# Performance work log

Measured on AMD Instinct MI355X. Metric: run time of the kernel, lower is better.

Reference implementation:

```python
import jax, jax.numpy as jnp
import numpy as np

LAMBDA_FGW = 0.5
TAU_KL = 0.1
N_OUTER = 5
N_SINKHORN = 10
DIM = 512


def _pdist(a, b):
    # sqrt(clamp(||a-b||^2, 1e-6)) computed via expansion (avoids BxKxMxD temp)
    n2 = ((a * a).sum(-1)[:, :, None] + (b * b).sum(-1)[:, None, :]
          - 2.0 * jnp.einsum('bkd,bmd->bkm', a, b))
    return jnp.sqrt(jnp.clip(n2, 1e-6, None))


def setup_inputs() -> dict:
    key = jax.random.key(0)
    ks = jax.random.split(key, 10)
    B, K, M, D = 256, 128, 128, DIM
    inp = {
        'sq': jax.random.normal(ks[0], (B, K, D), jnp.float32),
        'sr': jax.random.normal(ks[1], (B, M, D), jnp.float32),
        'mask_q': jax.random.uniform(ks[2], (B, K), jnp.float32),
        'mask_r': jax.random.uniform(ks[3], (B, M), jnp.float32),
        'centroids_q': jax.random.normal(ks[4], (B, K, D), jnp.float32),
        'centroids_r': jax.random.normal(ks[5], (B, M, D), jnp.float32),
        'W1': jax.random.normal(ks[6], (D, D), jnp.float32) * 0.02,
        'b1': jnp.zeros((D,), jnp.float32),
        'W2': jax.random.normal(ks[7], (D, D), jnp.float32) * 0.02,
        'b2': jnp.zeros((D,), jnp.float32),
        'log_eps': jnp.asarray(np.log(0.05), jnp.float32),
    }
    return inp


def reference(sq, sr, mask_q, mask_r, centroids_q, centroids_r, W1, b1, W2, b2, log_eps):
    proj = lambda x: jax.nn.relu(x @ W1 + b1) @ W2 + b2
    pq, pr = proj(sq), proj(sr)
    C = _pdist(pq, pr)                      # [B,K,M]
    Sq = _pdist(centroids_q, centroids_q)   # [B,K,K]
    Sr = _pdist(centroids_r, centroids_r)   # [B,M,M]

    mu = mask_q / (mask_q.sum(-1, keepdims=True) + 1e-8)  # [B,K]
    nu = mask_r / (mask_r.sum(-1, keepdims=True) + 1e-8)  # [B,M]
    T = mu[:, :, None] * nu[:, None, :]

    eps = jnp.clip(jnp.exp(log_eps), 0.01, 0.5)
    rho = TAU_KL / (TAU_KL + eps)
    log_mu = jnp.log(jnp.clip(mu, 1e-8, None))
    log_nu = jnp.log(jnp.clip(nu, 1e-8, None))
    Sq2, Sr2 = Sq * Sq, Sr * Sr

    C_fgw = C
    for _ in range(N_OUTER):
        t1 = jnp.einsum('bkl,bl->bk', Sq2, T.sum(2))[:, :, None]
        t2 = jnp.einsum('bm,bmn->bn', T.sum(1), Sr2)[:, None, :]
        L_gw = t1 + t2 - 2.0 * jnp.einsum('bkl,blm->bkm', Sq, jnp.einsum('blm,bmn->bln', T, Sr))
        C_fgw = (1.0 - LAMBDA_FGW) * C + LAMBDA_FGW * L_gw
        log_K = -C_fgw / eps
        log_u = jnp.zeros_like(mu)
        log_v = jnp.zeros_like(nu)
        for _ in range(N_SINKHORN):
            log_u = rho * (log_mu - jax.nn.logsumexp(log_K + log_v[:, None, :], axis=2))
            log_v = rho * (log_nu - jax.nn.logsumexp(log_K + log_u[:, :, None], axis=1))
        T = jnp.exp(log_u[:, :, None] + log_K + log_v[:, None, :])

    cost = (T * C_fgw).sum((-1, -2))
    similarity = jax.nn.sigmoid(-cost)
    return similarity, T, C, cost
```

## Files before the change

kernel.cpp:

```cpp
#include <hip/hip_runtime.h>
#include <math.h>

typedef unsigned short u16;
typedef __attribute__((ext_vector_type(4))) float f32x4;
typedef __attribute__((ext_vector_type(8))) short bf16x8;
typedef __attribute__((ext_vector_type(4))) unsigned short u16x4;
typedef __attribute__((ext_vector_type(8))) unsigned short u16x8;

#define DEVI static __device__ __forceinline__

DEVI float b2f(u16 u){ union{float f; unsigned i;} v; v.i = ((unsigned)u)<<16; return v.f; }
DEVI u16 f2b(float f){ union{float f; unsigned i;} v; v.f=f;
  unsigned r = v.i + 0x7fffu + ((v.i>>16)&1u); return (u16)(r>>16); }

DEVI void gload_lds16(const void* g, void* l){
  __builtin_amdgcn_global_load_lds((const __attribute__((address_space(1))) void*)g,
                                   (__attribute__((address_space(3))) void*)l, 16, 0, 0);
}

DEVI void lds_bar(){ asm volatile("s_waitcnt lgkmcnt(0)\n\ts_barrier" ::: "memory"); }

DEVI f32x4 vmax4(f32x4 a, f32x4 b){
  f32x4 r; r[0]=fmaxf(a[0],b[0]); r[1]=fmaxf(a[1],b[1]);
  r[2]=fmaxf(a[2],b[2]); r[3]=fmaxf(a[3],b[3]); return r;
}

__global__ void prologue_k(const float* __restrict__ W1, const float* __restrict__ W2,
                           u16* __restrict__ W1T, u16* __restrict__ W2T,
                           const float* __restrict__ mask_q, const float* __restrict__ mask_r,
                           float* __restrict__ lmu2, float* __restrict__ lnu2,
                           float* __restrict__ mu, float* __restrict__ nu){
  const int blk = blockIdx.x;
  if (blk < 2048){
    const float* W = (blk<1024)? W1 : W2;
    u16* Wt = (blk<1024)? W1T : W2T;
    int id = (blk&1023)*256 + threadIdx.x;
    int k = id>>9, c = id&511;
    Wt[c*512 + k] = f2b(W[id]);
  } else {
    __shared__ float red[2][4];
    const int h = threadIdx.x>>7, t = threadIdx.x&127;
    const int b = (blk-2048)*2 + h;
    float mq = mask_q[b*128+t], mr = mask_r[b*128+t];
    float s1 = mq, s2 = mr;
    #pragma unroll
    for (int off=1;off<64;off<<=1){ s1 += __shfl_xor(s1,off); s2 += __shfl_xor(s2,off); }
    if ((t&63)==0){ red[h][(t>>6)&1] = s1; red[h][2+((t>>6)&1)] = s2; }
    __syncthreads();
    float sumq = red[h][0]+red[h][1], sumr = red[h][2]+red[h][3];
    float muv = mq/(sumq+1e-8f), nuv = mr/(sumr+1e-8f);
    lmu2[b*128+t] = __log2f(fmaxf(muv,1e-8f));
    lnu2[b*128+t] = __log2f(fmaxf(nuv,1e-8f));
    mu[b*128+t] = muv;
    nu[b*128+t] = nuv;
  }
}

template<int ACT, int NORM, int AF32>
__global__ __launch_bounds__(256) void gemm_k(const u16* __restrict__ X,
    const float* __restrict__ Xf1, const float* __restrict__ Xf2,
    const u16* __restrict__ Wt, const float* __restrict__ bias, u16* __restrict__ OUT,
    float* __restrict__ NP4){
  __shared__ __align__(16) u16 smem[17920];
  u16* sA = smem;
  u16* sB = smem + 8192;
  const int tid = threadIdx.x, wave = tid>>6, lane = tid&63;
  const int bid = (blockIdx.x&7)*256 + (blockIdx.x>>3);
  const int rblk = bid>>2, cb = (bid&3)<<7;
  const u16* Xb = AF32 ? nullptr : (X + (size_t)rblk*(128*512));
  const float* Xbf = AF32 ? (rblk<256 ? Xf1 + (size_t)rblk*65536
                                      : Xf2 + (size_t)(rblk-256)*65536) : nullptr;
  const u16* Wb = Wt + (size_t)cb*512;
  const int lrow = lane&15, lg = lane>>4, wr = wave>>1, wc = wave&1;
  f32x4 acc[4][4] = {};
  for (int s=0;s<8;s++){
    const int k0 = s<<6;
    #pragma unroll
    for (int q=0;q<4;q++){
      const int i = (wave<<2)+q;
      const int row = (i<<3) + (lane>>3);
      const int cd = (lane&7) ^ (row&7);
      if (AF32){
        const float* src = Xbf + row*512 + k0 + (cd<<3);
        const f32x4 va = *(const f32x4*)src;
        const f32x4 vb = *(const f32x4*)(src+4);
        u16x8 t;
        #pragma unroll
        for (int e=0;e<4;e++){ t[e]=f2b(va[e]); t[4+e]=f2b(vb[e]); }
        *(u16x8*)((char*)sA + i*1024 + lane*16) = t;
      } else {
        gload_lds16(Xb + row*512 + k0 + (cd<<3), sA + i*512);
      }
      gload_lds16(Wb + row*512 + k0 + (cd<<3), sB + i*512);
    }
    __syncthreads();
    #pragma unroll
    for (int kh=0;kh<2;kh++){
      bf16x8 a_[4], b_[4];
      #pragma unroll
      for (int i=0;i<4;i++){
        const int ra = (wr<<6)+(i<<4)+lrow;
        a_[i] = *(const bf16x8*)(sA + ra*64 + ((((kh<<2)+lg)^(ra&7))<<3));
        const int rb = (wc<<6)+(i<<4)+lrow;
        b_[i] = *(const bf16x8*)(sB + rb*64 + ((((kh<<2)+lg)^(rb&7))<<3));
      }
      #pragma unroll
      for (int i=0;i<4;i++)
        #pragma unroll
        for (int j=0;j<4;j++)
          acc[i][j] = __builtin_amdgcn_mfma_f32_16x16x32_bf16(a_[i], b_[j], acc[i][j], 0,0,0);
    }
    __syncthreads();
  }
  #pragma unroll
  for (int j=0;j<4;j++){
    const int colb = (wc<<6) + (j<<4) + lrow;
    const float bv = bias[cb + colb];
    #pragma unroll
    for (int i=0;i<4;i++){
      const int rowb = (wr<<6)+(i<<4)+(lg<<2);
      #pragma unroll
      for (int r=0;r<4;r++){
        float v = acc[i][j][r] + bv;
        if (ACT) v = fmaxf(v, 0.f);
        smem[(rowb+r)*140 + colb] = f2b(v);
      }
    }
  }
  __syncthreads();
  const int chunk = lane&15, rql = lane>>4;
  float ns[8];
  #pragma unroll
  for (int it=0; it<8; it++){
    const int rowb = it*16 + wave*4 + rql;
    u16x8 v8 = *(const u16x8*)(smem + rowb*140 + chunk*8);
    *(u16x8*)(OUT + (size_t)((rblk<<7)+rowb)*512 + cb + chunk*8) = v8;
    if (NORM){
      float s = 0.f;
      #pragma unroll
      for (int e=0;e<8;e++){ float f = b2f(v8[e]); s = fmaf(f,f,s); }
      s += __shfl_xor(s,1); s += __shfl_xor(s,2);
      s += __shfl_xor(s,4); s += __shfl_xor(s,8);
      ns[it] = s;
    }
  }
  if (NORM && chunk==0){
    #pragma unroll
    for (int it=0;it<8;it++)
      NP4[(size_t)(bid&3)*65536 + (rblk<<7) + it*16 + wave*4 + rql] = ns[it];
  }
}

__global__ __launch_bounds__(256) void pdist_all_k(const u16* __restrict__ PQ,
    const float* __restrict__ NP4, const float* __restrict__ cq,
    const float* __restrict__ cr, float* __restrict__ Cm,
    char* __restrict__ SQHL, char* __restrict__ SRHL){
  __shared__ __align__(16) u16 sA[8192];
  __shared__ __align__(16) u16 sB[8192];
  __shared__ float nA[128], nB[128];
  const int tid = threadIdx.x, wave = tid>>6, lane = tid&63;
  const int lrow = lane&15, lg = lane>>4, wr = wave>>1, wc = wave&1;
  const int b = blockIdx.x & 255;

  if (blockIdx.x < 256){
    if (tid < 128){
      const int row = b*128 + tid;
      nA[tid] = NP4[row] + NP4[65536+row] + NP4[131072+row] + NP4[196608+row];
    } else {
      const int row = 32768 + b*128 + (tid-128);
      nB[tid-128] = NP4[row] + NP4[65536+row] + NP4[131072+row] + NP4[196608+row];
    }
    const u16* Ab = PQ + (size_t)b*(128*512);
    const u16* Bb = PQ + (size_t)(32768 + b*128)*512;
    f32x4 acc[4][4] = {};
    for (int s=0;s<8;s++){
      const int k0 = s<<6;
      #pragma unroll
      for (int q=0;q<4;q++){
        const int i = (wave<<2)+q;
        const int row = (i<<3) + (lane>>3);
        const int cd = (lane&7) ^ (row&7);
        gload_lds16(Ab + row*512 + k0 + (cd<<3), sA + i*512);
        gload_lds16(Bb + row*512 + k0 + (cd<<3), sB + i*512);
      }
      __syncthreads();
      #pragma unroll
      for (int kh=0;kh<2;kh++){
        bf16x8 a_[4], b_[4];
        #pragma unroll
        for (int i=0;i<4;i++){
          const int ra = (wr<<6)+(i<<4)+lrow;
          a_[i] = *(const bf16x8*)(sA + ra*64 + ((((kh<<2)+lg)^(ra&7))<<3));
          const int rb = (wc<<6)+(i<<4)+lrow;
          b_[i] = *(const bf16x8*)(sB + rb*64 + ((((kh<<2)+lg)^(rb&7))<<3));
        }
        #pragma unroll
        for (int i=0;i<4;i++)
          #pragma unroll
          for (int j=0;j<4;j++)
            acc[i][j] = __builtin_amdgcn_mfma_f32_16x16x32_bf16(a_[i], b_[j], acc[i][j], 0,0,0);
      }
      __syncthreads();
    }
    #pragma unroll
    for (int j=0;j<4;j++){
      const int col = (wc<<6)+(j<<4)+lrow;
      const float nbv = nB[col];
      #pragma unroll
      for (int i=0;i<4;i++){
        const int row0 = (wr<<6)+(i<<4)+(lg<<2);
        #pragma unroll
        for (int r=0;r<4;r++){
          float n2 = nA[row0+r] + nbv - 2.0f*acc[i][j][r];
          Cm[(size_t)b*16384 + (size_t)(row0+r)*128 + col] = sqrtf(fmaxf(n2, 1e-6f));
        }
      }
    }
  } else {
    const float* Sb = ((blockIdx.x < 512)? cq : cr) + (size_t)b*65536;
    char* SHL = (blockIdx.x < 512)? SQHL : SRHL;
    f32x4 acc[4][4] = {};
    float nacc[4] = {0.f,0.f,0.f,0.f};
    for (int s=0;s<8;s++){
      const int k0 = s<<6;
      #pragma unroll
      for (int q=0;q<4;q++){
        const int i = (wave<<2)+q;
        const int row = (i<<3) + (lane>>3);
        const int cd = (lane&7) ^ (row&7);
        const float* src = Sb + row*512 + k0 + (cd<<3);
        const f32x4 va = *(const f32x4*)src;
        const f32x4 vb = *(const f32x4*)(src+4);
        u16x8 t;
        #pragma unroll
        for (int e=0;e<4;e++){ t[e]=f2b(va[e]); t[4+e]=f2b(vb[e]); }
        #pragma unroll
        for (int e=0;e<8;e++){ float fv=b2f(t[e]); nacc[q]=fmaf(fv,fv,nacc[q]); }
        *(u16x8*)((char*)sA + i*1024 + lane*16) = t;
      }
      __syncthreads();
      #pragma unroll
      for (int kh=0;kh<2;kh++){
        bf16x8 a_[4], b_[4];
        #pragma unroll
        for (int i=0;i<4;i++){
          const int ra = (wr<<6)+(i<<4)+lrow;
          a_[i] = *(const bf16x8*)(sA + ra*64 + ((((kh<<2)+lg)^(ra&7))<<3));
          const int rb = (wc<<6)+(i<<4)+lrow;
          b_[i] = *(const bf16x8*)(sA + rb*64 + ((((kh<<2)+lg)^(rb&7))<<3));
        }
        #pragma unroll
        for (int i=0;i<4;i++)
          #pragma unroll
          for (int j=0;j<4;j++)
            acc[i][j] = __builtin_amdgcn_mfma_f32_16x16x32_bf16(a_[i], b_[j], acc[i][j], 0,0,0);
      }
      __syncthreads();
    }
    #pragma unroll
    for (int q=0;q<4;q++){
      float v = nacc[q];
      v += __shfl_xor(v,1); v += __shfl_xor(v,2); v += __shfl_xor(v,4);
      if ((lane&7)==0) nA[((wave<<2)+q)*8 + (lane>>3)] = v;
    }
    __syncthreads();
    #pragma unroll
    for (int j=0;j<4;j++){
      const int col = (wc<<6)+(j<<4)+lrow;
      const float nbv = nA[col];
      #pragma unroll
      for (int i=0;i<4;i++){
        const int row0 = (wr<<6)+(i<<4)+(lg<<2);
        u16x4 hi4, lo4;
        #pragma unroll
        for (int r=0;r<4;r++){
          float n2 = nA[row0+r] + nbv - 2.0f*acc[i][j][r];
          float sv = sqrtf(fmaxf(n2, 1e-6f));
          u16 h = f2b(sv); hi4[r] = h;
          lo4[r] = f2b(sv - b2f(h));
        }
        const int sa = col*256 + ((((row0>>3)^col)&15)<<4) + ((row0&7)<<1);
        char* base = SHL + (size_t)b*65536;
        *(u16x4*)(base + sa) = hi4;
        *(u16x4*)(base + 32768 + sa) = lo4;
      }
    }
  }
}

__global__ __launch_bounds__(512,1) void fgw_loop_k(
    const char* __restrict__ SQHL, const char* __restrict__ SRHL,
    const float* __restrict__ C_g,
    const float* __restrict__ MU, const float* __restrict__ NU,
    const float* __restrict__ LMU2, const float* __restrict__ LNU2,
    const float* __restrict__ log_eps,
    float* __restrict__ T_out, float* __restrict__ cost_out, float* __restrict__ sim_out)
{
  __shared__ __align__(16) char bufT[65536];
  __shared__ __align__(16) char bufS[65536];
  __shared__ __align__(16) float avs[128], bvs[128], t1s[128], t2s[128];
  __shared__ __align__(16) float lus[128], lvs[128];
  __shared__ float redc[8];

  const int b = blockIdx.x, tid = threadIdx.x;
  const int w = tid>>6, lane = tid&63, l15 = lane&15, lg = lane>>4;
  const char* SqHLb = SQHL + (size_t)b*65536;
  const char* SrHLb = SRHL + (size_t)b*65536;
  const float* Cb   = C_g + (size_t)b*16384;
  const float* MUb  = MU + b*128;
  const float* NUb  = NU + b*128;

  float eps = __expf(log_eps[0]); eps = fminf(fmaxf(eps,0.01f),0.5f);
  const float rho = 0.1f/(0.1f+eps);
  const float hscale = 0.5f*1.4426950408889634f/eps;

  const int kR = 16*w + l15;
  const int n0 = 16*w + 4*lg;
  const float lmu2R = LMU2[b*128+kR];
  const float lnu2C = LNU2[b*128+kR];

  const int rowA256 = (16*w + l15)*256;
  const int glo2 = lg ^ (l15 & 3);
  const int ghi2 = l15 & 12;
  const int wtail = l15*256 + ((((2*w + (lg>>1)) ^ l15)&15)<<4) + ((lg&1)<<3);
  const int slotW = lg*16 + (l15^lg);

  f32x4 Cf2[8];
  #pragma unroll
  for (int kt=0;kt<8;kt++)
    Cf2[kt] = -hscale * (*(const f32x4*)(Cb + (size_t)(16*kt+l15)*128 + n0));

  f32x4 lkR[8], lkC[8];
  float luR = 0.f, lvC = 0.f;

  #pragma unroll
  for (int r2=0;r2<8;r2++)
    gload_lds16(SrHLb + r2*8192 + tid*16, bufS + r2*8192 + tid*16);

  for (int outer=0; outer<5; outer++){
    {
      f32x4 avp = {0.f,0.f,0.f,0.f};
      #pragma unroll
      for (int q=0;q<8;q++){
        f32x4 TR;
        if (outer==0){
          const f32x4 nu4 = *(const f32x4*)(NUb + 16*q + 4*lg);
          TR = MUb[kR]*nu4;
        } else {
          const f32x4 lv4 = *(const f32x4*)&lvs[16*q + 4*lg];
          #pragma unroll
          for (int e=0;e<4;e++) TR[e] = exp2f(lkR[q][e] + luR + lv4[e]);
        }
        u16x4 hi4, lo4;
        #pragma unroll
        for (int e=0;e<4;e++){
          u16 h = f2b(TR[e]); hi4[e] = h;
          lo4[e] = f2b(TR[e] - b2f(h));
        }
        const int sa = kR*256 + ((((2*q+(lg>>1)) ^ l15)&15)<<4) + ((lg&1)<<3);
        *(u16x4*)(bufT + sa) = hi4;
        *(u16x4*)(bufT + 32768 + sa) = lo4;
        avp += TR;
      }
      float av = avp[0]+avp[1]+avp[2]+avp[3];
      av += __shfl_xor(av,16); av += __shfl_xor(av,32);
      if (lg==0){
        avs[kR] = av;
        bvs[kR] = (outer==0) ? NUb[kR] : exp2f(lnu2C - 10.f*eps*lvC);
      }
    }
    __syncthreads();

    {
      const int p = tid>>2, sub = tid&3;
      float s2 = 0.f;
      #pragma unroll
      for (int gg=0; gg<4; gg++){
        const int g = 4*sub+gg;
        const int off = p*256 + (((g ^ (p&15))&15)<<4);
        const u16x8 h8 = *(const u16x8*)(bufS + off);
        const u16x8 l8 = *(const u16x8*)(bufS + 32768 + off);
        const f32x4 bva = *(const f32x4*)&bvs[8*g];
        const f32x4 bvb = *(const f32x4*)&bvs[8*g+4];
        #pragma unroll
        for (int e=0;e<4;e++){
          float x = b2f(h8[e]) + b2f(l8[e]);
          s2 = fmaf(bva[e], x*x, s2);
          float y2 = b2f(h8[4+e]) + b2f(l8[4+e]);
          s2 = fmaf(bvb[e], y2*y2, s2);
        }
      }
      s2 += __shfl_xor(s2,1); s2 += __shfl_xor(s2,2);
      if (sub==0) t2s[p] = s2;
    }
    f32x4 acc1[8] = {};
    #pragma unroll
    for (int qt=0;qt<4;qt++){
      const int colOff = (((4*qt) ^ ghi2) | glo2) << 4;
      const bf16x8 ahi = *(const bf16x8*)(bufT + rowA256 + colOff);
      const bf16x8 alo = *(const bf16x8*)(bufT + 32768 + rowA256 + colOff);
      const int bbase = l15*256 + colOff;
      #pragma unroll
      for (int nt=0;nt<8;nt++){
        const bf16x8 bhi = *(const bf16x8*)(bufS + nt*4096 + bbase);
        const bf16x8 blo = *(const bf16x8*)(bufS + 32768 + nt*4096 + bbase);
        acc1[nt] = __builtin_amdgcn_mfma_f32_16x16x32_bf16(ahi, bhi, acc1[nt], 0,0,0);
        acc1[nt] = __builtin_amdgcn_mfma_f32_16x16x32_bf16(ahi, blo, acc1[nt], 0,0,0);
        acc1[nt] = __builtin_amdgcn_mfma_f32_16x16x32_bf16(alo, bhi, acc1[nt], 0,0,0);
      }
    }
    __syncthreads();

    #pragma unroll
    for (int r2=0;r2<8;r2++)
      gload_lds16(SqHLb + r2*8192 + tid*16, bufS + r2*8192 + tid*16);
    #pragma unroll
    for (int nt=0;nt<8;nt++){
      u16x4 hi4, lo4;
      #pragma unroll
      for (int r=0;r<4;r++){
        u16 h = f2b(acc1[nt][r]); hi4[r] = h;
        lo4[r] = f2b(acc1[nt][r] - b2f(h));
      }
      const int sa = nt*4096 + wtail;
      *(u16x4*)(bufT + sa) = hi4;
      *(u16x4*)(bufT + 32768 + sa) = lo4;
    }
    __syncthreads();

    {
      const int p = tid>>2, sub = tid&3;
      float s1 = 0.f;
      #pragma unroll
      for (int gg=0; gg<4; gg++){
        const int g = 4*sub+gg;
        const int off = p*256 + (((g ^ (p&15))&15)<<4);
        const u16x8 h8 = *(const u16x8*)(bufS + off);
        const u16x8 l8 = *(const u16x8*)(bufS + 32768 + off);
        const f32x4 ava = *(const f32x4*)&avs[8*g];
        const f32x4 avb = *(const f32x4*)&avs[8*g+4];
        #pragma unroll
        for (int e=0;e<4;e++){
          float x = b2f(h8[e]) + b2f(l8[e]);
          s1 = fmaf(ava[e], x*x, s1);
          float y2 = b2f(h8[4+e]) + b2f(l8[4+e]);
          s1 = fmaf(avb[e], y2*y2, s1);
        }
      }
      s1 += __shfl_xor(s1,1); s1 += __shfl_xor(s1,2);
      if (sub==0) t1s[p] = s1;
    }
    f32x4 acc2[8] = {};
    #pragma unroll
    for (int qt=0;qt<4;qt++){
      const int colOff = (((4*qt) ^ ghi2) | glo2) << 4;
      const bf16x8 ahi = *(const bf16x8*)(bufT + rowA256 + colOff);
      const bf16x8 alo = *(const bf16x8*)(bufT + 32768 + rowA256 + colOff);
      const int bbase = l15*256 + colOff;
      #pragma unroll
      for (int kt=0;kt<8;kt++){
        const bf16x8 bhi = *(const bf16x8*)(bufS + kt*4096 + bbase);
        const bf16x8 blo = *(const bf16x8*)(bufS + 32768 + kt*4096 + bbase);
        acc2[kt] = __builtin_amdgcn_mfma_f32_16x16x32_bf16(ahi, bhi, acc2[kt], 0,0,0);
        acc2[kt] = __builtin_amdgcn_mfma_f32_16x16x32_bf16(ahi, blo, acc2[kt], 0,0,0);
        acc2[kt] = __builtin_amdgcn_mfma_f32_16x16x32_bf16(alo, bhi, acc2[kt], 0,0,0);
      }
    }
    __syncthreads();

    if (outer<4){
      #pragma unroll
      for (int r2=0;r2<8;r2++)
        gload_lds16(SrHLb + r2*8192 + tid*16, bufS + r2*8192 + tid*16);
    }
    f32x4 lkf[8];
    {
      const f32x4 t24 = *(const f32x4*)&t2s[n0];
      #pragma unroll
      for (int kt=0;kt<8;kt++){
        const float t1v = t1s[16*kt+l15];
        lkf[kt] = Cf2[kt] + hscale*(2.0f*acc2[kt] - t1v - t24);
      }
    }
    #pragma unroll
    for (int kt=0;kt<8;kt++)
      *(f32x4*)(bufT + (((kt*8+w)*64 + slotW)<<4)) = lkf[kt];
    lds_bar();
    #pragma unroll
    for (int q=0;q<8;q++)
      lkR[q] = *(const f32x4*)(bufT + (((w*8+q)*64 + slotW)<<4));
    #pragma unroll
    for (int q=0;q<8;q++){
      #pragma unroll
      for (int e=0;e<4;e++){
        const int slotC = (l15>>2)*16 + ((4*lg+e) ^ (l15>>2));
        lkC[q][e] = *(const float*)(bufT + (((q*8+w)*64 + slotC)<<4) + ((l15&3)<<2));
      }
    }

    for (int it=0; it<10; it++){
      f32x4 y[8];
      #pragma unroll
      for (int q=0;q<8;q++){
        y[q] = lkR[q];
        if (it) y[q] += *(const f32x4*)&lvs[16*q+4*lg];
      }
      f32x4 m4 = vmax4(vmax4(vmax4(y[0],y[1]),vmax4(y[2],y[3])),
                       vmax4(vmax4(y[4],y[5]),vmax4(y[6],y[7])));
      float mx = fmaxf(fmaxf(m4[0],m4[1]), fmaxf(m4[2],m4[3]));
      mx = fmaxf(mx,__shfl_xor(mx,16)); mx = fmaxf(mx,__shfl_xor(mx,32));
      f32x4 s4 = {0.f,0.f,0.f,0.f};
      #pragma unroll
      for (int q=0;q<8;q++){
        #pragma unroll
        for (int e=0;e<4;e++) s4[e] += exp2f(y[q][e]-mx);
      }
      float s = s4[0]+s4[1]+s4[2]+s4[3];
      s += __shfl_xor(s,16); s += __shfl_xor(s,32);
      luR = rho*(lmu2R - (mx + __log2f(s)));
      if (lg==0) lus[kR] = luR;
      lds_bar();
      #pragma unroll
      for (int q=0;q<8;q++)
        y[q] = lkC[q] + *(const f32x4*)&lus[16*q+4*lg];
      m4 = vmax4(vmax4(vmax4(y[0],y[1]),vmax4(y[2],y[3])),
                 vmax4(vmax4(y[4],y[5]),vmax4(y[6],y[7])));
      mx = fmaxf(fmaxf(m4[0],m4[1]), fmaxf(m4[2],m4[3]));
      mx = fmaxf(mx,__shfl_xor(mx,16)); mx = fmaxf(mx,__shfl_xor(mx,32));
      s4 = (f32x4){0.f,0.f,0.f,0.f};
      #pragma unroll
      for (int q=0;q<8;q++){
        #pragma unroll
        for (int e=0;e<4;e++) s4[e] += exp2f(y[q][e]-mx);
      }
      s = s4[0]+s4[1]+s4[2]+s4[3];
      s += __shfl_xor(s,16); s += __shfl_xor(s,32);
      lvC = rho*(lnu2C - (mx + __log2f(s)));
      if (lg==0) lvs[kR] = lvC;
      lds_bar();
    }

    if (outer==4){
      float cp = 0.f;
      float* Tb = T_out + (size_t)b*16384;
      #pragma unroll
      for (int q=0;q<8;q++){
        const f32x4 lv4 = *(const f32x4*)&lvs[16*q+4*lg];
        f32x4 t;
        #pragma unroll
        for (int e=0;e<4;e++) t[e] = exp2f(lkR[q][e] + luR + lv4[e]);
        *(f32x4*)(Tb + kR*128 + 16*q + 4*lg) = t;
        const f32x4 pr = t*lkR[q];
        cp += pr[0]+pr[1]+pr[2]+pr[3];
      }
      cp *= -eps*0.6931471805599453f;
      #pragma unroll
      for (int off=1;off<64;off<<=1) cp += __shfl_xor(cp, off);
      if (lane==0) redc[w] = cp;
      __syncthreads();
      if (tid==0){
        float tot = 0.f;
        #pragma unroll
        for (int w2=0;w2<8;w2++) tot += redc[w2];
        cost_out[b] = tot;
        sim_out[b]  = 1.0f/(1.0f + __expf(tot));
      }
    }
  }
}

extern "C" void kernel_launch(void* const* d_in, const int* in_sizes, int n_in,
                              void* d_out, int out_size, void* d_ws, size_t ws_size,
                              hipStream_t stream){
  const float* sq      = (const float*)d_in[0];
  const float* sr      = (const float*)d_in[1];
  const float* mask_q  = (const float*)d_in[2];
  const float* mask_r  = (const float*)d_in[3];
  const float* cq      = (const float*)d_in[4];
  const float* cr      = (const float*)d_in[5];
  const float* W1      = (const float*)d_in[6];
  const float* b1      = (const float*)d_in[7];
  const float* W2      = (const float*)d_in[8];
  const float* b2      = (const float*)d_in[9];
  const float* log_eps = (const float*)d_in[10];

  float* out  = (float*)d_out;
  float* sim  = out;
  float* Tm   = out + 256;
  float* Cm   = Tm + 4194304;
  float* cost = Cm + 4194304;

  char* ws = (char*)d_ws;
  size_t off = 0;
  auto alloc = [&](size_t bytes)->void*{ void* p = ws + off; off += (bytes+255)&~(size_t)255; return p; };
  u16*   PQ  = (u16*)  alloc(67108864);
  u16*   HQ  = (u16*)  alloc(67108864);
  u16*   W1T = (u16*)  alloc(524288);
  u16*   W2T = (u16*)  alloc(524288);
  float* NP4 = (float*)alloc(1048576);
  float* LMU = (float*)alloc(131072);
  float* LNU = (float*)alloc(131072);
  float* MUA = (float*)alloc(131072);
  float* NUA = (float*)alloc(131072);
  (void)ws_size; (void)in_sizes; (void)n_in; (void)out_size;

  char* SQHL = (char*)PQ;
  char* SRHL = (char*)PQ + 16777216;

  prologue_k<<<2176,256,0,stream>>>(W1, W2, W1T, W2T, mask_q, mask_r,
                                    LMU, LNU, MUA, NUA);
  gemm_k<1,0,1><<<2048,256,0,stream>>>(nullptr, sq, sr, W1T, b1, HQ, nullptr);
  gemm_k<0,1,0><<<2048,256,0,stream>>>(HQ, nullptr, nullptr, W2T, b2, PQ, NP4);
  pdist_all_k<<<768,256,0,stream>>>(PQ, NP4, cq, cr, Cm, SQHL, SRHL);
  fgw_loop_k<<<256,512,0,stream>>>(SQHL, SRHL, Cm, MUA, NUA, LMU, LNU,
                                   log_eps, Tm, cost, sim);
}
```

Baseline: 412.9 us.

## Double fgw_loop block to 1024 threads, halving per-wave tile work

```diff
diff --git a/kernel.cpp b/kernel.cpp
--- a/kernel.cpp
+++ b/kernel.cpp
@@ -288,7 +288,7 @@
   }
 }
 
-__global__ __launch_bounds__(512,1) void fgw_loop_k(
+__global__ __launch_bounds__(1024,1) void fgw_loop_k(
     const char* __restrict__ SQHL, const char* __restrict__ SRHL,
     const float* __restrict__ C_g,
     const float* __restrict__ MU, const float* __restrict__ NU,
@@ -300,10 +300,12 @@
   __shared__ __align__(16) char bufS[65536];
   __shared__ __align__(16) float avs[128], bvs[128], t1s[128], t2s[128];
   __shared__ __align__(16) float lus[128], lvs[128];
-  __shared__ float redc[8];
+  __shared__ float redc[16];
 
   const int b = blockIdx.x, tid = threadIdx.x;
   const int w = tid>>6, lane = tid&63, l15 = lane&15, lg = lane>>4;
+  const int l7 = lane&7, p8 = lane>>3;
+  const int at = w>>1, par = w&1;
   const char* SqHLb = SQHL + (size_t)b*65536;
   const char* SrHLb = SRHL + (size_t)b*65536;
   const float* Cb   = C_g + (size_t)b*16384;
@@ -314,42 +316,40 @@
   const float rho = 0.1f/(0.1f+eps);
   const float hscale = 0.5f*1.4426950408889634f/eps;
 
-  const int kR = 16*w + l15;
-  const int n0 = 16*w + 4*lg;
+  const int kR = 8*w + l7;
   const float lmu2R = LMU2[b*128+kR];
   const float lnu2C = LNU2[b*128+kR];
 
-  const int rowA256 = (16*w + l15)*256;
+  const int rowA256 = (16*at + l15)*256;
   const int glo2 = lg ^ (l15 & 3);
   const int ghi2 = l15 & 12;
-  const int wtail = l15*256 + ((((2*w + (lg>>1)) ^ l15)&15)<<4) + ((lg&1)<<3);
-  const int slotW = lg*16 + (l15^lg);
-
-  f32x4 Cf2[8];
+  const int wtail = l15*256 + ((((2*at + (lg>>1)) ^ l15)&15)<<4) + ((lg&1)<<3);
+
+  f32x4 Cf2[4];
   #pragma unroll
-  for (int kt=0;kt<8;kt++)
-    Cf2[kt] = -hscale * (*(const f32x4*)(Cb + (size_t)(16*kt+l15)*128 + n0));
-
-  f32x4 lkR[8], lkC[8];
+  for (int j=0;j<4;j++)
+    Cf2[j] = -hscale * (*(const f32x4*)(Cb + (size_t)(16*(4*par+j)+l15)*128 + 16*at + 4*lg));
+
+  f32x4 lkR[4], lkC[4];
   float luR = 0.f, lvC = 0.f;
 
   #pragma unroll
-  for (int r2=0;r2<8;r2++)
-    gload_lds16(SrHLb + r2*8192 + tid*16, bufS + r2*8192 + tid*16);
+  for (int r2=0;r2<4;r2++)
+    gload_lds16(SrHLb + r2*16384 + tid*16, bufS + r2*16384 + tid*16);
 
   for (int outer=0; outer<5; outer++){
     {
       f32x4 avp = {0.f,0.f,0.f,0.f};
       #pragma unroll
-      for (int q=0;q<8;q++){
+      for (int jj=0;jj<4;jj++){
         f32x4 TR;
         if (outer==0){
-          const f32x4 nu4 = *(const f32x4*)(NUb + 16*q + 4*lg);
+          const f32x4 nu4 = *(const f32x4*)(NUb + 16*p8 + 4*jj);
           TR = MUb[kR]*nu4;
         } else {
-          const f32x4 lv4 = *(const f32x4*)&lvs[16*q + 4*lg];
+          const f32x4 lv4 = *(const f32x4*)&lvs[16*p8 + 4*jj];
           #pragma unroll
-          for (int e=0;e<4;e++) TR[e] = exp2f(lkR[q][e] + luR + lv4[e]);
+          for (int e=0;e<4;e++) TR[e] = exp2f(lkR[jj][e] + luR + lv4[e]);
         }
         u16x4 hi4, lo4;
         #pragma unroll
@@ -357,14 +357,14 @@
           u16 h = f2b(TR[e]); hi4[e] = h;
           lo4[e] = f2b(TR[e] - b2f(h));
         }
-        const int sa = kR*256 + ((((2*q+(lg>>1)) ^ l15)&15)<<4) + ((lg&1)<<3);
+        const int sa = kR*256 + ((((2*p8+(jj>>1)) ^ (kR&15))&15)<<4) + ((jj&1)<<3);
         *(u16x4*)(bufT + sa) = hi4;
         *(u16x4*)(bufT + 32768 + sa) = lo4;
         avp += TR;
       }
       float av = avp[0]+avp[1]+avp[2]+avp[3];
-      av += __shfl_xor(av,16); av += __shfl_xor(av,32);
-      if (lg==0){
+      av += __shfl_xor(av,8); av += __shfl_xor(av,16); av += __shfl_xor(av,32);
+      if (p8==0){
         avs[kR] = av;
         bvs[kR] = (outer==0) ? NUb[kR] : exp2f(lnu2C - 10.f*eps*lvC);
       }
@@ -372,11 +372,11 @@
     __syncthreads();
 
     {
-      const int p = tid>>2, sub = tid&3;
+      const int p = 8*w + p8, sub = l7;
       float s2 = 0.f;
       #pragma unroll
-      for (int gg=0; gg<4; gg++){
-        const int g = 4*sub+gg;
+      for (int gg=0; gg<2; gg++){
+        const int g = 2*sub+gg;
         const int off = p*256 + (((g ^ (p&15))&15)<<4);
         const u16x8 h8 = *(const u16x8*)(bufS + off);
         const u16x8 l8 = *(const u16x8*)(bufS + 32768 + off);
@@ -390,50 +390,50 @@
           s2 = fmaf(bvb[e], y2*y2, s2);
         }
       }
-      s2 += __shfl_xor(s2,1); s2 += __shfl_xor(s2,2);
+      s2 += __shfl_xor(s2,1); s2 += __shfl_xor(s2,2); s2 += __shfl_xor(s2,4);
       if (sub==0) t2s[p] = s2;
     }
-    f32x4 acc1[8] = {};
+    f32x4 acc1[4] = {};
     #pragma unroll
     for (int qt=0;qt<4;qt++){
       const int colOff = (((4*qt) ^ ghi2) | glo2) << 4;
       const bf16x8 ahi = *(const bf16x8*)(bufT + rowA256 + colOff);
       const bf16x8 alo = *(const bf16x8*)(bufT + 32768 + rowA256 + colOff);
-      const int bbase = l15*256 + colOff;
-      #pragma unroll
-      for (int nt=0;nt<8;nt++){
-        const bf16x8 bhi = *(const bf16x8*)(bufS + nt*4096 + bbase);
-        const bf16x8 blo = *(const bf16x8*)(bufS + 32768 + nt*4096 + bbase);
-        acc1[nt] = __builtin_amdgcn_mfma_f32_16x16x32_bf16(ahi, bhi, acc1[nt], 0,0,0);
-        acc1[nt] = __builtin_amdgcn_mfma_f32_16x16x32_bf16(ahi, blo, acc1[nt], 0,0,0);
-        acc1[nt] = __builtin_amdgcn_mfma_f32_16x16x32_bf16(alo, bhi, acc1[nt], 0,0,0);
-      }
-    }
-    __syncthreads();
-
-    #pragma unroll
-    for (int r2=0;r2<8;r2++)
-      gload_lds16(SqHLb + r2*8192 + tid*16, bufS + r2*8192 + tid*16);
-    #pragma unroll
-    for (int nt=0;nt<8;nt++){
+      #pragma unroll
+      for (int j=0;j<4;j++){
+        const int boff = (4*par+j)*4096 + l15*256 + colOff;
+        const bf16x8 bhi = *(const bf16x8*)(bufS + boff);
+        const bf16x8 blo = *(const bf16x8*)(bufS + 32768 + boff);
+        acc1[j] = __builtin_amdgcn_mfma_f32_16x16x32_bf16(ahi, bhi, acc1[j], 0,0,0);
+        acc1[j] = __builtin_amdgcn_mfma_f32_16x16x32_bf16(ahi, blo, acc1[j], 0,0,0);
+        acc1[j] = __builtin_amdgcn_mfma_f32_16x16x32_bf16(alo, bhi, acc1[j], 0,0,0);
+      }
+    }
+    __syncthreads();
+
+    #pragma unroll
+    for (int r2=0;r2<4;r2++)
+      gload_lds16(SqHLb + r2*16384 + tid*16, bufS + r2*16384 + tid*16);
+    #pragma unroll
+    for (int j=0;j<4;j++){
       u16x4 hi4, lo4;
       #pragma unroll
       for (int r=0;r<4;r++){
-        u16 h = f2b(acc1[nt][r]); hi4[r] = h;
-        lo4[r] = f2b(acc1[nt][r] - b2f(h));
-      }
-      const int sa = nt*4096 + wtail;
+        u16 h = f2b(acc1[j][r]); hi4[r] = h;
+        lo4[r] = f2b(acc1[j][r] - b2f(h));
+      }
+      const int sa = (4*par+j)*4096 + wtail;
       *(u16x4*)(bufT + sa) = hi4;
       *(u16x4*)(bufT + 32768 + sa) = lo4;
     }
     __syncthreads();
 
     {
-      const int p = tid>>2, sub = tid&3;
+      const int p = 8*w + p8, sub = l7;
       float s1 = 0.f;
       #pragma unroll
-      for (int gg=0; gg<4; gg++){
-        const int g = 4*sub+gg;
+      for (int gg=0; gg<2; gg++){
+        const int g = 2*sub+gg;
         const int off = p*256 + (((g ^ (p&15))&15)<<4);
         const u16x8 h8 = *(const u16x8*)(bufS + off);
         const u16x8 l8 = *(const u16x8*)(bufS + 32768 + off);
@@ -447,96 +447,99 @@
           s1 = fmaf(avb[e], y2*y2, s1);
         }
       }
-      s1 += __shfl_xor(s1,1); s1 += __shfl_xor(s1,2);
+      s1 += __shfl_xor(s1,1); s1 += __shfl_xor(s1,2); s1 += __shfl_xor(s1,4);
       if (sub==0) t1s[p] = s1;
     }
-    f32x4 acc2[8] = {};
+    f32x4 acc2[4] = {};
     #pragma unroll
     for (int qt=0;qt<4;qt++){
       const int colOff = (((4*qt) ^ ghi2) | glo2) << 4;
       const bf16x8 ahi = *(const bf16x8*)(bufT + rowA256 + colOff);
       const bf16x8 alo = *(const bf16x8*)(bufT + 32768 + rowA256 + colOff);
-      const int bbase = l15*256 + colOff;
-      #pragma unroll
-      for (int kt=0;kt<8;kt++){
-        const bf16x8 bhi = *(const bf16x8*)(bufS + kt*4096 + bbase);
-        const bf16x8 blo = *(const bf16x8*)(bufS + 32768 + kt*4096 + bbase);
-        acc2[kt] = __builtin_amdgcn_mfma_f32_16x16x32_bf16(ahi, bhi, acc2[kt], 0,0,0);
-        acc2[kt] = __builtin_amdgcn_mfma_f32_16x16x32_bf16(ahi, blo, acc2[kt], 0,0,0);
-        acc2[kt] = __builtin_amdgcn_mfma_f32_16x16x32_bf16(alo, bhi, acc2[kt], 0,0,0);
+      #pragma unroll
+      for (int j=0;j<4;j++){
+        const int boff = (4*par+j)*4096 + l15*256 + colOff;
+        const bf16x8 bhi = *(const bf16x8*)(bufS + boff);
+        const bf16x8 blo = *(const bf16x8*)(bufS + 32768 + boff);
+        acc2[j] = __builtin_amdgcn_mfma_f32_16x16x32_bf16(ahi, bhi, acc2[j], 0,0,0);
+        acc2[j] = __builtin_amdgcn_mfma_f32_16x16x32_bf16(ahi, blo, acc2[j], 0,0,0);
+        acc2[j] = __builtin_amdgcn_mfma_f32_16x16x32_bf16(alo, bhi, acc2[j], 0,0,0);
       }
     }
     __syncthreads();
 
     if (outer<4){
       #pragma unroll
-      for (int r2=0;r2<8;r2++)
-        gload_lds16(SrHLb + r2*8192 + tid*16, bufS + r2*8192 + tid*16);
-    }
-    f32x4 lkf[8];
+      for (int r2=0;r2<4;r2++)
+        gload_lds16(SrHLb + r2*16384 + tid*16, bufS + r2*16384 + tid*16);
+    }
+    f32x4 lkf[4];
     {
-      const f32x4 t24 = *(const f32x4*)&t2s[n0];
-      #pragma unroll
-      for (int kt=0;kt<8;kt++){
-        const float t1v = t1s[16*kt+l15];
-        lkf[kt] = Cf2[kt] + hscale*(2.0f*acc2[kt] - t1v - t24);
-      }
-    }
-    #pragma unroll
-    for (int kt=0;kt<8;kt++)
-      *(f32x4*)(bufT + (((kt*8+w)*64 + slotW)<<4)) = lkf[kt];
+      const f32x4 t24 = *(const f32x4*)&t2s[16*at + 4*lg];
+      #pragma unroll
+      for (int j=0;j<4;j++){
+        const float t1v = t1s[16*(4*par+j)+l15];
+        lkf[j] = Cf2[j] + hscale*(2.0f*acc2[j] - t1v - t24);
+      }
+    }
+    #pragma unroll
+    for (int j=0;j<4;j++){
+      const int row = 16*(4*par+j)+l15;
+      *(f32x4*)(bufT + (size_t)(row*32 + (((4*at+lg) ^ (row&31))&31))*16) = lkf[j];
+    }
     lds_bar();
     #pragma unroll
-    for (int q=0;q<8;q++)
-      lkR[q] = *(const f32x4*)(bufT + (((w*8+q)*64 + slotW)<<4));
-    #pragma unroll
-    for (int q=0;q<8;q++){
+    for (int jj=0;jj<4;jj++)
+      lkR[jj] = *(const f32x4*)(bufT + (size_t)(kR*32 + (((4*p8+jj) ^ (kR&31))&31))*16);
+    #pragma unroll
+    for (int jj=0;jj<4;jj++){
       #pragma unroll
       for (int e=0;e<4;e++){
-        const int slotC = (l15>>2)*16 + ((4*lg+e) ^ (l15>>2));
-        lkC[q][e] = *(const float*)(bufT + (((q*8+w)*64 + slotC)<<4) + ((l15&3)<<2));
+        const int row = 16*p8 + 4*jj + e;
+        lkC[jj][e] = *(const float*)(bufT
+            + (size_t)(row*32 + (((kR>>2) ^ (row&31))&31))*16 + (kR&3)*4);
       }
     }
 
     for (int it=0; it<10; it++){
-      f32x4 y[8];
-      #pragma unroll
-      for (int q=0;q<8;q++){
-        y[q] = lkR[q];
-        if (it) y[q] += *(const f32x4*)&lvs[16*q+4*lg];
-      }
-      f32x4 m4 = vmax4(vmax4(vmax4(y[0],y[1]),vmax4(y[2],y[3])),
-                       vmax4(vmax4(y[4],y[5]),vmax4(y[6],y[7])));
+      f32x4 y[4];
+      #pragma unroll
+      for (int jj=0;jj<4;jj++){
+        y[jj] = lkR[jj];
+        if (it) y[jj] += *(const f32x4*)&lvs[16*p8+4*jj];
+      }
+      f32x4 m4 = vmax4(vmax4(y[0],y[1]), vmax4(y[2],y[3]));
       float mx = fmaxf(fmaxf(m4[0],m4[1]), fmaxf(m4[2],m4[3]));
-      mx = fmaxf(mx,__shfl_xor(mx,16)); mx = fmaxf(mx,__shfl_xor(mx,32));
+      mx = fmaxf(mx,__shfl_xor(mx,8)); mx = fmaxf(mx,__shfl_xor(mx,16));
+      mx = fmaxf(mx,__shfl_xor(mx,32));
       f32x4 s4 = {0.f,0.f,0.f,0.f};
       #pragma unroll
-      for (int q=0;q<8;q++){
-        #pragma unroll
-        for (int e=0;e<4;e++) s4[e] += exp2f(y[q][e]-mx);
+      for (int jj=0;jj<4;jj++){
+        #pragma unroll
+        for (int e=0;e<4;e++) s4[e] += exp2f(y[jj][e]-mx);
       }
       float s = s4[0]+s4[1]+s4[2]+s4[3];
-      s += __shfl_xor(s,16); s += __shfl_xor(s,32);
+      s += __shfl_xor(s,8); s += __shfl_xor(s,16); s += __shfl_xor(s,32);
       luR = rho*(lmu2R - (mx + __log2f(s)));
-      if (lg==0) lus[kR] = luR;
+      if (p8==0) lus[kR] = luR;
       lds_bar();
       #pragma unroll
-      for (int q=0;q<8;q++)
-        y[q] = lkC[q] + *(const f32x4*)&lus[16*q+4*lg];
-      m4 = vmax4(vmax4(vmax4(y[0],y[1]),vmax4(y[2],y[3])),
-                 vmax4(vmax4(y[4],y[5]),vmax4(y[6],y[7])));
+      for (int jj=0;jj<4;jj++)
+        y[jj] = lkC[jj] + *(const f32x4*)&lus[16*p8+4*jj];
+      m4 = vmax4(vmax4(y[0],y[1]), vmax4(y[2],y[3]));
       mx = fmaxf(fmaxf(m4[0],m4[1]), fmaxf(m4[2],m4[3]));
-      mx = fmaxf(mx,__shfl_xor(mx,16)); mx = fmaxf(mx,__shfl_xor(mx,32));
+      mx = fmaxf(mx,__shfl_xor(mx,8)); mx = fmaxf(mx,__shfl_xor(mx,16));
+      mx = fmaxf(mx,__shfl_xor(mx,32));
       s4 = (f32x4){0.f,0.f,0.f,0.f};
       #pragma unroll
-      for (int q=0;q<8;q++){
-        #pragma unroll
-        for (int e=0;e<4;e++) s4[e] += exp2f(y[q][e]-mx);
+      for (int jj=0;jj<4;jj++){
+        #pragma unroll
+        for (int e=0;e<4;e++) s4[e] += exp2f(y[jj][e]-mx);
       }
       s = s4[0]+s4[1]+s4[2]+s4[3];
-      s += __shfl_xor(s,16); s += __shfl_xor(s,32);
+      s += __shfl_xor(s,8); s += __shfl_xor(s,16); s += __shfl_xor(s,32);
       lvC = rho*(lnu2C - (mx + __log2f(s)));
-      if (lg==0) lvs[kR] = lvC;
+      if (p8==0) lvs[kR] = lvC;
       lds_bar();
     }
 
@@ -544,13 +547,13 @@
       float cp = 0.f;
       float* Tb = T_out + (size_t)b*16384;
       #pragma unroll
-      for (int q=0;q<8;q++){
-        const f32x4 lv4 = *(const f32x4*)&lvs[16*q+4*lg];
+      for (int jj=0;jj<4;jj++){
+        const f32x4 lv4 = *(const f32x4*)&lvs[16*p8+4*jj];
         f32x4 t;
         #pragma unroll
-        for (int e=0;e<4;e++) t[e] = exp2f(lkR[q][e] + luR + lv4[e]);
-        *(f32x4*)(Tb + kR*128 + 16*q + 4*lg) = t;
-        const f32x4 pr = t*lkR[q];
+        for (int e=0;e<4;e++) t[e] = exp2f(lkR[jj][e] + luR + lv4[e]);
+        *(f32x4*)(Tb + kR*128 + 16*p8 + 4*jj) = t;
+        const f32x4 pr = t*lkR[jj];
         cp += pr[0]+pr[1]+pr[2]+pr[3];
       }
       cp *= -eps*0.6931471805599453f;
@@ -561,7 +564,7 @@
       if (tid==0){
         float tot = 0.f;
         #pragma unroll
-        for (int w2=0;w2<8;w2++) tot += redc[w2];
+        for (int w2=0;w2<16;w2++) tot += redc[w2];
         cost_out[b] = tot;
         sim_out[b]  = 1.0f/(1.0f + __expf(tot));
       }
@@ -612,6 +615,6 @@
   gemm_k<1,0,1><<<2048,256,0,stream>>>(nullptr, sq, sr, W1T, b1, HQ, nullptr);
   gemm_k<0,1,0><<<2048,256,0,stream>>>(HQ, nullptr, nullptr, W2T, b2, PQ, NP4);
   pdist_all_k<<<768,256,0,stream>>>(PQ, NP4, cq, cr, Cm, SQHL, SRHL);
-  fgw_loop_k<<<256,512,0,stream>>>(SQHL, SRHL, Cm, MUA, NUA, LMU, LNU,
-                                   log_eps, Tm, cost, sim);
+  fgw_loop_k<<<256,1024,0,stream>>>(SQHL, SRHL, Cm, MUA, NUA, LMU, LNU,
+                                    log_eps, Tm, cost, sim);
 }
```

Result: no change. 417.4 us (+1.1%).
